# Performance work log

Hardware: AMD Instinct MI355X
Metric: run time of the kernel (lower is better)

Reference implementation:

```python
import jax, jax.numpy as jnp
import numpy as np

EMBED_DIM = 64
NUM_HEADS = 8
D_K = EMBED_DIM // NUM_HEADS  # 8
B, S = 8, 1024


def setup_inputs() -> dict:
    key = jax.random.key(0)
    ks = jax.random.split(key, 10)
    f32 = jnp.float32
    lim = 1.0 / np.sqrt(EMBED_DIM)
    def lin(k):
        kw, kb = jax.random.split(k)
        w = jax.random.uniform(kw, (EMBED_DIM, EMBED_DIM), f32, -lim, lim)
        b = jax.random.uniform(kb, (EMBED_DIM,), f32, -lim, lim)
        return w, b
    wq, bq = lin(ks[0])
    wk, bk = lin(ks[1])
    wv, bv = lin(ks[2])
    wo, bo = lin(ks[3])
    theta = jax.random.normal(ks[4], (EMBED_DIM,), f32)  # trainable RY angles, one per wire
    x = jax.random.normal(ks[5], (B, S, EMBED_DIM), f32)
    return {"x": x, "wq": wq, "bq": bq, "wk": wk, "bk": bk,
            "wv": wv, "bv": bv, "theta": theta, "wo": wo, "bo": bo}


def _quantum_map(t, theta):
    # Per-qubit circuit on |0>: RX(t_i) encode, RY(theta_i), <PauliZ_i>.
    # Product state => <Z_i> = cos(theta_i) * cos(t_i) exactly.
    return jnp.cos(theta) * jnp.cos(t.reshape(-1, EMBED_DIM))  # [N, E]


def reference(x, wq, bq, wk, bk, wv, bv, theta, wo, bo):
    # Linear QKV (torch nn.Linear: x @ W^T + b)
    q = x @ wq.T + bq
    k = x @ wk.T + bk
    v = x @ wv.T + bv
    # Quantum measurement map, flattened over batch*seq (as in the original)
    q_q = _quantum_map(q, theta)  # [N, E], N = B*S
    k_q = _quantum_map(k, theta)
    v_q = _quantum_map(v, theta)
    # Full flattened attention: [N, N] scores (original never reshapes back)
    scores = (q_q @ k_q.T) / jnp.sqrt(jnp.asarray(D_K, x.dtype))
    attn = jax.nn.softmax(scores, axis=-1)  # dropout is identity in eval
    out = attn @ v_q  # [N, E]
    return out @ wo.T + bo
```

## Files before the change

kernel.cpp:

```cpp
#include <hip/hip_runtime.h>
#include <hip/hip_bf16.h>

#define NQ 8192
#define DIM 64
#define SPLITS 16
#define QBLK 128
#define WQ 64
#define BN 64
#define KEYS_PER_SPLIT (NQ / SPLITS)
#define NTILES (KEYS_PER_SPLIT / BN)
#define GRID_FLASH ((NQ / QBLK) * SPLITS)
#define MERGEB 512
#define MROWS (NQ / MERGEB)
#define SC2 0.51012301920911057f
#define KSTR 72

typedef short s8v __attribute__((ext_vector_type(8)));
typedef short s4v __attribute__((ext_vector_type(4)));
typedef float f4v __attribute__((ext_vector_type(4)));
typedef int   i4v __attribute__((ext_vector_type(4)));

__device__ __forceinline__ float b2f(short s) {
  unsigned int u = ((unsigned int)(unsigned short)s) << 16;
  return __uint_as_float(u);
}
__device__ __forceinline__ short f2b(float f) {
  __hip_bfloat16 h = __float2bfloat16(f);
  return *reinterpret_cast<short*>(&h);
}
__device__ __forceinline__ int pack_bf16x2(float a, float b) {
  union { __hip_bfloat162 h; int i; } u;
  u.h = __float22bfloat162_rn(make_float2(a, b));
  return u.i;
}
__device__ __forceinline__ float fast_exp2(float x) {
#if __has_builtin(__builtin_amdgcn_exp2f)
  return __builtin_amdgcn_exp2f(x);
#else
  return exp2f(x);
#endif
}

#define QKV_TPB 128
#define QKV_ROWS 32
__global__ __launch_bounds__(128) void qkv_kernel(
    const float* __restrict__ x,
    const float* __restrict__ wq, const float* __restrict__ bq,
    const float* __restrict__ wk, const float* __restrict__ bk,
    const float* __restrict__ wv, const float* __restrict__ bv,
    const float* __restrict__ theta,
    short* __restrict__ qq, short* __restrict__ kvT) {
  __shared__ __align__(16) short wsh[3 * DIM][KSTR];
  __shared__ __align__(16) short xsb[QKV_ROWS][KSTR];
  __shared__ __align__(16) float bb[3 * DIM];
  __shared__ __align__(16) float ctl[DIM];
  int tid = threadIdx.x;
  for (int i = tid; i < 3 * DIM * 16; i += QKV_TPB) {
    int m = i >> 10;
    int rem = i & 1023;
    int r = rem >> 4, c4 = (rem & 15) << 2;
    const float* src = (m == 0) ? wq : (m == 1) ? wk : wv;
    float4 w = *(const float4*)&src[r * DIM + c4];
    s4v p = {f2b(w.x), f2b(w.y), f2b(w.z), f2b(w.w)};
    *(s4v*)&wsh[m * DIM + r][c4] = p;
  }
  int rowbase = blockIdx.x * QKV_ROWS;
  for (int i = tid; i < QKV_ROWS * 16; i += QKV_TPB) {
    int r = i >> 4, c4 = (i & 15) << 2;
    float4 v = *(const float4*)&x[(rowbase + r) * DIM + c4];
    s4v p = {f2b(v.x), f2b(v.y), f2b(v.z), f2b(v.w)};
    *(s4v*)&xsb[r][c4] = p;
  }
  if (tid < DIM) {
    ctl[tid] = __cosf(theta[tid]);
    bb[tid] = bq[tid];
    bb[DIM + tid] = bk[tid];
    bb[2 * DIM + tid] = bv[tid];
  }
  __syncthreads();

  int wave = tid >> 6, lane = tid & 63;
  int l15 = lane & 15, quad = lane >> 4;
  int n = rowbase + wave * 16 + l15;

  s8v xf0 = *(const s8v*)&xsb[wave * 16 + l15][quad * 8];
  s8v xf1 = *(const s8v*)&xsb[wave * 16 + l15][quad * 8 + 32];

  size_t tb = (size_t)(n >> 6) * 8192;
  int nperm = (n & 3) | ((n & 16) >> 2);
  size_t vbase = tb + 4096 + ((n & 32) >> 5) * 2048 + ((n & 15) >> 2) * 128 + nperm;

#pragma unroll
  for (int mt = 0; mt < 12; ++mt) {
    s8v wf0 = *(const s8v*)&wsh[mt * 16 + l15][quad * 8];
    s8v wf1 = *(const s8v*)&wsh[mt * 16 + l15][quad * 8 + 32];
    f4v acc = (f4v){0.f, 0.f, 0.f, 0.f};
    acc = __builtin_amdgcn_mfma_f32_16x16x32_bf16(wf0, xf0, acc, 0, 0, 0);
    acc = __builtin_amdgcn_mfma_f32_16x16x32_bf16(wf1, xf1, acc, 0, 0, 0);
    int d0 = mt * 16 + quad * 4;
    float4 bias = *(const float4*)&bb[d0];
    float4 ct4 = *(const float4*)&ctl[d0 & 63];
    float y0 = __cosf(acc[0] + bias.x) * ct4.x;
    float y1 = __cosf(acc[1] + bias.y) * ct4.y;
    float y2 = __cosf(acc[2] + bias.z) * ct4.z;
    float y3 = __cosf(acc[3] + bias.w) * ct4.w;
    if (mt < 4) {
      s4v p = {f2b(SC2 * y0), f2b(SC2 * y1), f2b(SC2 * y2), f2b(SC2 * y3)};
      *(s4v*)&qq[(size_t)n * DIM + d0] = p;
    } else if (mt < 8) {
      int e = d0 - 64;
      size_t idx = tb + ((n & 63) >> 4) * 1024 + (e >> 5) * 512 +
                   ((e & 31) >> 3) * 128 + (n & 15) * 8 + (e & 7);
      s4v p = {f2b(y0), f2b(y1), f2b(y2), f2b(y3)};
      *(s4v*)&kvT[idx] = p;
    } else {
      int e0 = d0 - 128;
      float ys[4] = {y0, y1, y2, y3};
#pragma unroll
      for (int r = 0; r < 4; ++r) {
        int e = e0 + r;
        kvT[vbase + (e >> 4) * 512 + (e & 15) * 8] = f2b(ys[r]);
      }
    }
  }
}

#if __has_builtin(__builtin_amdgcn_global_load_lds)
#define DMA_CHUNK(srcp, dstp) \
  __builtin_amdgcn_global_load_lds( \
      (const __attribute__((address_space(1))) void*)(srcp), \
      (__attribute__((address_space(3))) void*)(dstp), 16, 0, 0)
#else
#define DMA_CHUNK(srcp, dstp) \
  { *(s8v*)((short*)(dstp) + (threadIdx.x & 63) * 8) = \
        *(const s8v*)((const short*)(srcp)); }
#endif

__global__ __launch_bounds__(128, 2) void flash_kernel(
    const short* __restrict__ qq, const short* __restrict__ kvT,
    short* __restrict__ pO, short* __restrict__ pL) {
  __shared__ __align__(16) short lds[2][8192];

  int tid = threadIdx.x;
  int wave = tid >> 6, lane = tid & 63;
  int l15 = lane & 15, quad = lane >> 4;
  int qblock = blockIdx.x >> 4, split = blockIdx.x & 15;
  int qbase = qblock * QBLK + wave * WQ;

  s8v qf[4][2];
#pragma unroll
  for (int qt = 0; qt < 4; ++qt) {
    const short* qr = qq + (qbase + qt * 16 + l15) * DIM + quad * 8;
    qf[qt][0] = *(const s8v*)qr;
    qf[qt][1] = *(const s8v*)(qr + 32);
  }

  const short ONE = (short)0x3F80;
  const s8v ones = {ONE, ONE, ONE, ONE, ONE, ONE, ONE, ONE};

  f4v o[4][4], ol[4];
#pragma unroll
  for (int qt = 0; qt < 4; ++qt) {
    ol[qt] = (f4v){0.f, 0.f, 0.f, 0.f};
#pragma unroll
    for (int c = 0; c < 4; ++c) o[qt][c] = (f4v){0.f, 0.f, 0.f, 0.f};
  }

  int gt0 = split * NTILES;

#define STAGE(T, BUF)                                                        \
  {                                                                          \
    const short* s_ = kvT + (size_t)(gt0 + (T)) * 8192 + wave * 4096 +       \
                      lane * 8;                                              \
    short* d_ = &lds[BUF][wave * 4096];                                      \
    _Pragma("unroll") for (int c2 = 0; c2 < 8; ++c2)                         \
        DMA_CHUNK(s_ + c2 * 512, d_ + c2 * 512);                             \
  }

  STAGE(0, 0)

  for (int t = 0; t < NTILES; ++t) {
    __syncthreads();
    if (t + 1 < NTILES) STAGE(t + 1, (t + 1) & 1)

    const short* kb = lds[t & 1];
    const short* vb = lds[t & 1] + 4096;

#pragma unroll
    for (int kp = 0; kp < 2; ++kp) {
      i4v pai[4];
#pragma unroll
      for (int h = 0; h < 2; ++h) {
        int kt = kp * 2 + h;
        s8v kf0 = *(const s8v*)&kb[(kt * 2) * 512 + lane * 8];
        s8v kf1 = *(const s8v*)&kb[(kt * 2 + 1) * 512 + lane * 8];
#pragma unroll
        for (int qt = 0; qt < 4; ++qt) {
          f4v acc = (f4v){0.f, 0.f, 0.f, 0.f};
          acc = __builtin_amdgcn_mfma_f32_16x16x32_bf16(kf0, qf[qt][0], acc, 0, 0, 0);
          acc = __builtin_amdgcn_mfma_f32_16x16x32_bf16(kf1, qf[qt][1], acc, 0, 0, 0);
          pai[qt][h * 2]     = pack_bf16x2(fast_exp2(acc[0]), fast_exp2(acc[1]));
          pai[qt][h * 2 + 1] = pack_bf16x2(fast_exp2(acc[2]), fast_exp2(acc[3]));
        }
      }
#pragma unroll
      for (int qt = 0; qt < 4; ++qt)
        ol[qt] = __builtin_amdgcn_mfma_f32_16x16x32_bf16(
            __builtin_bit_cast(s8v, pai[qt]), ones, ol[qt], 0, 0, 0);
#pragma unroll
      for (int c = 0; c < 4; ++c) {
        s8v vf = *(const s8v*)&vb[(kp * 4 + c) * 512 + lane * 8];
#pragma unroll
        for (int qt = 0; qt < 4; ++qt)
          o[qt][c] = __builtin_amdgcn_mfma_f32_16x16x32_bf16(
              __builtin_bit_cast(s8v, pai[qt]), vf, o[qt][c], 0, 0, 0);
      }
    }
  }

#pragma unroll
  for (int qt = 0; qt < 4; ++qt) {
#pragma unroll
    for (int r = 0; r < 4; ++r) {
      int q = qbase + qt * 16 + quad * 4 + r;
      short* dst = pO + (size_t)q * (SPLITS * DIM) + split * DIM;
#pragma unroll
      for (int c = 0; c < 4; ++c) dst[c * 16 + l15] = f2b(o[qt][c][r]);
      if (l15 == 0) pL[(size_t)q * SPLITS + split] = f2b(ol[qt][r]);
    }
  }
}

__global__ __launch_bounds__(256) void merge_kernel(
    const short* __restrict__ pO, const short* __restrict__ pL,
    const float* __restrict__ wo, const float* __restrict__ bo,
    float* __restrict__ out) {
  __shared__ __align__(16) short wsh[DIM * KSTR];
  __shared__ __align__(16) float att[MROWS * DIM];
  int tid = threadIdx.x;
  int q0 = blockIdx.x * MROWS;
  for (int i = tid; i < DIM * 16; i += 256) {
    int r = i >> 4, c4 = (i & 15) << 2;
    float4 w = *(const float4*)&wo[r * DIM + c4];
    s4v p = {f2b(w.x), f2b(w.y), f2b(w.z), f2b(w.w)};
    *(s4v*)&wsh[r * KSTR + c4] = p;
  }
  int wave = tid >> 6, j = tid & 63;
#pragma unroll
  for (int i = 0; i < MROWS / 4; ++i) {
    int rr = wave * (MROWS / 4) + i;
    int q = q0 + rr;
    const short* prow = pO + (size_t)q * (SPLITS * DIM);
    s8v v0 = *(const s8v*)&prow[j * 8];
    s8v v1 = *(const s8v*)&prow[512 + j * 8];
    float a[8];
#pragma unroll
    for (int m = 0; m < 8; ++m) a[m] = b2f(v0[m]) + b2f(v1[m]);
#pragma unroll
    for (int st = 8; st < 64; st <<= 1)
#pragma unroll
      for (int m = 0; m < 8; ++m) a[m] += __shfl_xor(a[m], st);
    const short* lrow = pL + (size_t)q * SPLITS;
    s8v lv0 = *(const s8v*)&lrow[0];
    s8v lv1 = *(const s8v*)&lrow[8];
    float l = 0.f;
#pragma unroll
    for (int m = 0; m < 8; ++m) l += b2f(lv0[m]) + b2f(lv1[m]);
#if __has_builtin(__builtin_amdgcn_rcpf)
    float ri = __builtin_amdgcn_rcpf(l);
#else
    float ri = 1.f / l;
#endif
    if (j < 8) {
      float4 f0 = {a[0] * ri, a[1] * ri, a[2] * ri, a[3] * ri};
      float4 f1 = {a[4] * ri, a[5] * ri, a[6] * ri, a[7] * ri};
      *(float4*)&att[rr * DIM + j * 8] = f0;
      *(float4*)&att[rr * DIM + j * 8 + 4] = f1;
    }
  }
  __syncthreads();
  int e = tid & 63, rg = tid >> 6;
  for (int rr = rg; rr < MROWS; rr += 4) {
    float acc = bo[e];
#pragma unroll
    for (int c8 = 0; c8 < 8; ++c8) {
      s8v w = *(const s8v*)&wsh[e * KSTR + c8 * 8];
      const float* ar = &att[rr * DIM + c8 * 8];
      acc += ar[0] * b2f(w[0]) + ar[1] * b2f(w[1]) + ar[2] * b2f(w[2]) + ar[3] * b2f(w[3])
           + ar[4] * b2f(w[4]) + ar[5] * b2f(w[5]) + ar[6] * b2f(w[6]) + ar[7] * b2f(w[7]);
    }
    out[(size_t)(q0 + rr) * DIM + e] = acc;
  }
}

extern "C" void kernel_launch(void* const* d_in, const int* in_sizes, int n_in,
                              void* d_out, int out_size, void* d_ws, size_t ws_size,
                              hipStream_t stream) {
  const float* x  = (const float*)d_in[0];
  const float* wq = (const float*)d_in[1];
  const float* bq = (const float*)d_in[2];
  const float* wk = (const float*)d_in[3];
  const float* bk = (const float*)d_in[4];
  const float* wv = (const float*)d_in[5];
  const float* bv = (const float*)d_in[6];
  const float* th = (const float*)d_in[7];
  const float* wo = (const float*)d_in[8];
  const float* bo = (const float*)d_in[9];

  char* ws = (char*)d_ws;
  short* qq  = (short*)(ws);
  short* kvT = (short*)(ws + (1u << 20));
  short* pO  = (short*)(ws + (3u << 20));
  short* pL  = (short*)(ws + (19u << 20));

  hipLaunchKernelGGL(qkv_kernel, dim3(NQ / QKV_ROWS), dim3(QKV_TPB), 0, stream,
                     x, wq, bq, wk, bk, wv, bv, th, qq, kvT);
  hipLaunchKernelGGL(flash_kernel, dim3(GRID_FLASH), dim3(128), 0, stream,
                     qq, kvT, pO, pL);
  hipLaunchKernelGGL(merge_kernel, dim3(MERGEB), dim3(256), 0, stream,
                     pO, pL, wo, bo, (float*)d_out);
}
```

Baseline: 120.9 us.

## Drop LDS staging and load K/V tiles directly from global per wave

Flash kernel now uses single-wave blocks of 64 query rows that read K and V fragments straight from global memory instead of staging them into double-buffered LDS via async DMA. This removes the per-tile __syncthreads and the LDS round-trip, and lets more blocks reside per CU. In exchange, the K/V tiles are no longer shared between waves, so global/L2 read traffic doubles and load latency is exposed directly to the MFMA loop.

Result: slower. 134.2 us (+11.0%).

```diff
diff --git a/kernel.cpp b/kernel.cpp
--- a/kernel.cpp
+++ b/kernel.cpp
@@ -4,8 +4,7 @@
 #define NQ 8192
 #define DIM 64
 #define SPLITS 16
-#define QBLK 128
-#define WQ 64
+#define QBLK 64
 #define BN 64
 #define KEYS_PER_SPLIT (NQ / SPLITS)
 #define NTILES (KEYS_PER_SPLIT / BN)
@@ -125,27 +124,13 @@
   }
 }
 
-#if __has_builtin(__builtin_amdgcn_global_load_lds)
-#define DMA_CHUNK(srcp, dstp) \
-  __builtin_amdgcn_global_load_lds( \
-      (const __attribute__((address_space(1))) void*)(srcp), \
-      (__attribute__((address_space(3))) void*)(dstp), 16, 0, 0)
-#else
-#define DMA_CHUNK(srcp, dstp) \
-  { *(s8v*)((short*)(dstp) + (threadIdx.x & 63) * 8) = \
-        *(const s8v*)((const short*)(srcp)); }
-#endif
-
-__global__ __launch_bounds__(128, 2) void flash_kernel(
+__global__ __launch_bounds__(64, 3) void flash_kernel(
     const short* __restrict__ qq, const short* __restrict__ kvT,
     short* __restrict__ pO, short* __restrict__ pL) {
-  __shared__ __align__(16) short lds[2][8192];
-
-  int tid = threadIdx.x;
-  int wave = tid >> 6, lane = tid & 63;
+  int lane = threadIdx.x & 63;
   int l15 = lane & 15, quad = lane >> 4;
   int qblock = blockIdx.x >> 4, split = blockIdx.x & 15;
-  int qbase = qblock * QBLK + wave * WQ;
+  int qbase = qblock * QBLK;
 
   s8v qf[4][2];
 #pragma unroll
@@ -166,25 +151,10 @@
     for (int c = 0; c < 4; ++c) o[qt][c] = (f4v){0.f, 0.f, 0.f, 0.f};
   }
 
-  int gt0 = split * NTILES;
-
-#define STAGE(T, BUF)                                                        \
-  {                                                                          \
-    const short* s_ = kvT + (size_t)(gt0 + (T)) * 8192 + wave * 4096 +       \
-                      lane * 8;                                              \
-    short* d_ = &lds[BUF][wave * 4096];                                      \
-    _Pragma("unroll") for (int c2 = 0; c2 < 8; ++c2)                         \
-        DMA_CHUNK(s_ + c2 * 512, d_ + c2 * 512);                             \
-  }
-
-  STAGE(0, 0)
+  const short* kv0 = kvT + (size_t)(split * NTILES) * 8192 + lane * 8;
 
   for (int t = 0; t < NTILES; ++t) {
-    __syncthreads();
-    if (t + 1 < NTILES) STAGE(t + 1, (t + 1) & 1)
-
-    const short* kb = lds[t & 1];
-    const short* vb = lds[t & 1] + 4096;
+    const short* tb = kv0 + t * 8192;
 
 #pragma unroll
     for (int kp = 0; kp < 2; ++kp) {
@@ -192,8 +162,8 @@
 #pragma unroll
       for (int h = 0; h < 2; ++h) {
         int kt = kp * 2 + h;
-        s8v kf0 = *(const s8v*)&kb[(kt * 2) * 512 + lane * 8];
-        s8v kf1 = *(const s8v*)&kb[(kt * 2 + 1) * 512 + lane * 8];
+        s8v kf0 = *(const s8v*)(tb + (kt * 2) * 512);
+        s8v kf1 = *(const s8v*)(tb + (kt * 2 + 1) * 512);
 #pragma unroll
         for (int qt = 0; qt < 4; ++qt) {
           f4v acc = (f4v){0.f, 0.f, 0.f, 0.f};
@@ -209,7 +179,7 @@
             __builtin_bit_cast(s8v, pai[qt]), ones, ol[qt], 0, 0, 0);
 #pragma unroll
       for (int c = 0; c < 4; ++c) {
-        s8v vf = *(const s8v*)&vb[(kp * 4 + c) * 512 + lane * 8];
+        s8v vf = *(const s8v*)(tb + 4096 + (kp * 4 + c) * 512);
 #pragma unroll
         for (int qt = 0; qt < 4; ++qt)
           o[qt][c] = __builtin_amdgcn_mfma_f32_16x16x32_bf16(
@@ -315,7 +285,7 @@
 
   hipLaunchKernelGGL(qkv_kernel, dim3(NQ / QKV_ROWS), dim3(QKV_TPB), 0, stream,
                      x, wq, bq, wk, bk, wv, bv, th, qq, kvT);
-  hipLaunchKernelGGL(flash_kernel, dim3(GRID_FLASH), dim3(128), 0, stream,
+  hipLaunchKernelGGL(flash_kernel, dim3(GRID_FLASH), dim3(QBLK), 0, stream,
                      qq, kvT, pO, pL);
   hipLaunchKernelGGL(merge_kernel, dim3(MERGEB), dim3(256), 0, stream,
                      pO, pL, wo, bo, (float*)d_out);
```

## Pre-pack QKV weights into MFMA fragment layout in a separate prep kernel

Applied to the files above, without the earlier changes.

Adds a single-block prep kernel that converts the Q/K/V weights to bf16 in MFMA fragment order and stores the biases and cos(theta) in workspace. The QKV kernel then drops its shared-memory staging and barrier, reads weight fragments and x rows straight from global memory, and spreads the three projections over a second grid dimension with one-wave blocks. This removes the redundant per-block weight conversion and LDS traffic. In exchange it costs an extra kernel launch and three times as many reads of x.

Result: faster. 117.8 us (-2.6%).

```diff
diff --git a/kernel.cpp b/kernel.cpp
--- a/kernel.cpp
+++ b/kernel.cpp
@@ -41,73 +41,78 @@
 #endif
 }
 
-#define QKV_TPB 128
-#define QKV_ROWS 32
-__global__ __launch_bounds__(128) void qkv_kernel(
-    const float* __restrict__ x,
+__global__ __launch_bounds__(256) void prep_kernel(
     const float* __restrict__ wq, const float* __restrict__ bq,
     const float* __restrict__ wk, const float* __restrict__ bk,
     const float* __restrict__ wv, const float* __restrict__ bv,
     const float* __restrict__ theta,
+    short* __restrict__ wT, float* __restrict__ bbs, float* __restrict__ ctl) {
+  int t = threadIdx.x;
+#pragma unroll
+  for (int i = 0; i < 6; ++i) {
+    int g = t + 256 * i;
+    int c = g >> 6;
+    int lane = g & 63;
+    int mt = c >> 1, h = c & 1;
+    int l15 = lane & 15, quad = lane >> 4;
+    int srow = mt * 16 + l15;
+    int scol = h * 32 + quad * 8;
+    const float* src = (srow < 64) ? (wq + srow * DIM)
+                     : (srow < 128) ? (wk + (srow - 64) * DIM)
+                                    : (wv + (srow - 128) * DIM);
+    float4 a = *(const float4*)&src[scol];
+    float4 b = *(const float4*)&src[scol + 4];
+    s8v p = {f2b(a.x), f2b(a.y), f2b(a.z), f2b(a.w),
+             f2b(b.x), f2b(b.y), f2b(b.z), f2b(b.w)};
+    *(s8v*)&wT[g * 8] = p;
+  }
+  if (t < 192) bbs[t] = (t < 64) ? bq[t] : (t < 128) ? bk[t - 64] : bv[t - 128];
+  if (t < 64) ctl[t] = __cosf(theta[t]);
+}
+
+__global__ __launch_bounds__(64) void qkv_kernel(
+    const float* __restrict__ x, const short* __restrict__ wT,
+    const float* __restrict__ bbs, const float* __restrict__ ctl,
     short* __restrict__ qq, short* __restrict__ kvT) {
-  __shared__ __align__(16) short wsh[3 * DIM][KSTR];
-  __shared__ __align__(16) short xsb[QKV_ROWS][KSTR];
-  __shared__ __align__(16) float bb[3 * DIM];
-  __shared__ __align__(16) float ctl[DIM];
-  int tid = threadIdx.x;
-  for (int i = tid; i < 3 * DIM * 16; i += QKV_TPB) {
-    int m = i >> 10;
-    int rem = i & 1023;
-    int r = rem >> 4, c4 = (rem & 15) << 2;
-    const float* src = (m == 0) ? wq : (m == 1) ? wk : wv;
-    float4 w = *(const float4*)&src[r * DIM + c4];
-    s4v p = {f2b(w.x), f2b(w.y), f2b(w.z), f2b(w.w)};
-    *(s4v*)&wsh[m * DIM + r][c4] = p;
-  }
-  int rowbase = blockIdx.x * QKV_ROWS;
-  for (int i = tid; i < QKV_ROWS * 16; i += QKV_TPB) {
-    int r = i >> 4, c4 = (i & 15) << 2;
-    float4 v = *(const float4*)&x[(rowbase + r) * DIM + c4];
-    s4v p = {f2b(v.x), f2b(v.y), f2b(v.z), f2b(v.w)};
-    *(s4v*)&xsb[r][c4] = p;
-  }
-  if (tid < DIM) {
-    ctl[tid] = __cosf(theta[tid]);
-    bb[tid] = bq[tid];
-    bb[DIM + tid] = bk[tid];
-    bb[2 * DIM + tid] = bv[tid];
-  }
-  __syncthreads();
-
-  int wave = tid >> 6, lane = tid & 63;
+  int lane = threadIdx.x & 63;
   int l15 = lane & 15, quad = lane >> 4;
-  int n = rowbase + wave * 16 + l15;
-
-  s8v xf0 = *(const s8v*)&xsb[wave * 16 + l15][quad * 8];
-  s8v xf1 = *(const s8v*)&xsb[wave * 16 + l15][quad * 8 + 32];
+  int tg = blockIdx.x;
+  int mg = blockIdx.y;
+  int n = tg * 16 + l15;
+
+  const float* xr = x + (size_t)n * DIM + quad * 8;
+  float4 x0 = *(const float4*)&xr[0];
+  float4 x1 = *(const float4*)&xr[4];
+  float4 x2 = *(const float4*)&xr[32];
+  float4 x3 = *(const float4*)&xr[36];
+  s8v xf0 = {f2b(x0.x), f2b(x0.y), f2b(x0.z), f2b(x0.w),
+             f2b(x1.x), f2b(x1.y), f2b(x1.z), f2b(x1.w)};
+  s8v xf1 = {f2b(x2.x), f2b(x2.y), f2b(x2.z), f2b(x2.w),
+             f2b(x3.x), f2b(x3.y), f2b(x3.z), f2b(x3.w)};
 
   size_t tb = (size_t)(n >> 6) * 8192;
   int nperm = (n & 3) | ((n & 16) >> 2);
   size_t vbase = tb + 4096 + ((n & 32) >> 5) * 2048 + ((n & 15) >> 2) * 128 + nperm;
 
 #pragma unroll
-  for (int mt = 0; mt < 12; ++mt) {
-    s8v wf0 = *(const s8v*)&wsh[mt * 16 + l15][quad * 8];
-    s8v wf1 = *(const s8v*)&wsh[mt * 16 + l15][quad * 8 + 32];
+  for (int i = 0; i < 4; ++i) {
+    int mt = mg * 4 + i;
+    s8v wf0 = *(const s8v*)&wT[(mt * 2) * 512 + lane * 8];
+    s8v wf1 = *(const s8v*)&wT[(mt * 2 + 1) * 512 + lane * 8];
     f4v acc = (f4v){0.f, 0.f, 0.f, 0.f};
     acc = __builtin_amdgcn_mfma_f32_16x16x32_bf16(wf0, xf0, acc, 0, 0, 0);
     acc = __builtin_amdgcn_mfma_f32_16x16x32_bf16(wf1, xf1, acc, 0, 0, 0);
     int d0 = mt * 16 + quad * 4;
-    float4 bias = *(const float4*)&bb[d0];
+    float4 bias = *(const float4*)&bbs[d0];
     float4 ct4 = *(const float4*)&ctl[d0 & 63];
     float y0 = __cosf(acc[0] + bias.x) * ct4.x;
     float y1 = __cosf(acc[1] + bias.y) * ct4.y;
     float y2 = __cosf(acc[2] + bias.z) * ct4.z;
     float y3 = __cosf(acc[3] + bias.w) * ct4.w;
-    if (mt < 4) {
+    if (mg == 0) {
       s4v p = {f2b(SC2 * y0), f2b(SC2 * y1), f2b(SC2 * y2), f2b(SC2 * y3)};
       *(s4v*)&qq[(size_t)n * DIM + d0] = p;
-    } else if (mt < 8) {
+    } else if (mg == 1) {
       int e = d0 - 64;
       size_t idx = tb + ((n & 63) >> 4) * 1024 + (e >> 5) * 512 +
                    ((e & 31) >> 3) * 128 + (n & 15) * 8 + (e & 7);
@@ -312,9 +317,14 @@
   short* kvT = (short*)(ws + (1u << 20));
   short* pO  = (short*)(ws + (3u << 20));
   short* pL  = (short*)(ws + (19u << 20));
-
-  hipLaunchKernelGGL(qkv_kernel, dim3(NQ / QKV_ROWS), dim3(QKV_TPB), 0, stream,
-                     x, wq, bq, wk, bk, wv, bv, th, qq, kvT);
+  short* wT  = (short*)(ws + (20u << 20));
+  float* bbs = (float*)(ws + (20u << 20) + (48u << 10));
+  float* ctl = (float*)(ws + (20u << 20) + (52u << 10));
+
+  hipLaunchKernelGGL(prep_kernel, dim3(1), dim3(256), 0, stream,
+                     wq, bq, wk, bk, wv, bv, th, wT, bbs, ctl);
+  hipLaunchKernelGGL(qkv_kernel, dim3(NQ / 16, 3), dim3(64), 0, stream,
+                     x, wT, bbs, ctl, qq, kvT);
   hipLaunchKernelGGL(flash_kernel, dim3(GRID_FLASH), dim3(128), 0, stream,
                      qq, kvT, pO, pL);
   hipLaunchKernelGGL(merge_kernel, dim3(MERGEB), dim3(256), 0, stream,
```
